# Kernel optimization log

Hardware: AMD Instinct MI355X
Metric: run time of the kernel (lower is better)

The kernel has to match this reference:

```python
import jax, jax.numpy as jnp
import numpy as np

D_MODEL = 1024
D_FF = 4096


def _layernorm(x, gamma, beta, eps=1e-5):
    mu = jnp.mean(x, axis=-1, keepdims=True)
    var = jnp.var(x, axis=-1, keepdims=True)
    return (x - mu) * jax.lax.rsqrt(var + eps) * gamma + beta


def setup_inputs() -> dict:
    key = jax.random.key(0)
    ks = jax.random.split(key, 7)
    B, S = 4, 2048
    src = jax.random.normal(ks[0], (B, S, D_MODEL), dtype=jnp.float32)
    gamma1 = jnp.ones((D_MODEL,), jnp.float32)
    beta1 = jnp.zeros((D_MODEL,), jnp.float32)
    gamma2 = jnp.ones((D_MODEL,), jnp.float32)
    beta2 = jnp.zeros((D_MODEL,), jnp.float32)
    w1 = jax.random.normal(ks[1], (D_MODEL, D_FF), jnp.float32) * (1.0 / np.sqrt(D_MODEL))
    b1 = jnp.zeros((D_FF,), jnp.float32)
    w2 = jax.random.normal(ks[2], (D_FF, D_MODEL), jnp.float32) * (1.0 / np.sqrt(D_FF))
    b2 = jnp.zeros((D_MODEL,), jnp.float32)
    return {"src": src, "gamma1": gamma1, "beta1": beta1,
            "gamma2": gamma2, "beta2": beta2,
            "w1": w1, "b1": b1, "w2": w2, "b2": b2}


def reference(src, gamma1, beta1, gamma2, beta2, w1, b1, w2, b2):
    # Pre-LN self-attention (single head, Q=K=V=norm_x, no projections)
    norm_x = _layernorm(src, gamma1, beta1)
    dim_k = norm_x.shape[-1]
    scores = jnp.einsum('bqd,bkd->bqk', norm_x, norm_x) / jnp.sqrt(jnp.float32(dim_k))
    weights = jax.nn.softmax(scores, axis=-1)
    attn = jnp.einsum('bqk,bkd->bqd', weights, norm_x)
    x = src + attn  # dropout p=0 -> identity
    # Pre-LN FFN
    h = _layernorm(x, gamma2, beta2)
    h = jax.nn.gelu(h @ w1 + b1, approximate=False)
    h = h @ w2 + b2
    return h + x
```

## Files before the change

### kernel.cpp

```cpp
#include <hip/hip_runtime.h>
#include <hip/hip_bf16.h>
#include <math.h>

typedef __attribute__((ext_vector_type(8))) short s8vec;
typedef __attribute__((ext_vector_type(16))) float f32x16;
typedef __attribute__((ext_vector_type(4))) unsigned short us4;
typedef __attribute__((ext_vector_type(2))) unsigned short us2;

__device__ __forceinline__ unsigned short f2bf(float f) {
  unsigned u = __float_as_uint(f);
  u = (u + 0x7fffu + ((u >> 16) & 1u)) >> 16;
  return (unsigned short)u;
}
__device__ __forceinline__ float bf2f(unsigned short u) {
  return __uint_as_float(((unsigned)u) << 16);
}

__device__ __forceinline__ float fast_gelu(float t) {
  float t2 = t * t;
  float u = t * (1.59576912f + 0.07135481f * t2);
  float e = __expf(-u);
  return t * __frcp_rn(1.0f + e);
}

__device__ __forceinline__ void async_ld16(const unsigned short* g, unsigned short* l) {
  __builtin_amdgcn_global_load_lds(
      (__attribute__((address_space(1))) void*)g,
      (__attribute__((address_space(3))) void*)l, 16, 0, 0);
}

template <int EPI>
__global__ __launch_bounds__(256) void gemm_nt(
    const unsigned short* __restrict__ A, const unsigned short* __restrict__ B,
    float* __restrict__ outF, unsigned short* __restrict__ outB,
    const float* __restrict__ bias, const float* __restrict__ res,
    int M, int N, int K,
    long long bA, long long bB, long long bO, long long bR, float scale)
{
  __shared__ __align__(16) unsigned short As[128 * 64];
  __shared__ __align__(16) unsigned short Bs[128 * 64];

  const int tid = threadIdx.x;
  const int w = tid >> 6;
  const int l = tid & 63;
  const int z = blockIdx.z;

  A += (size_t)z * bA;
  B += (size_t)z * bB;

  const size_t tileM = (size_t)blockIdx.y * 128;
  const size_t tileN = (size_t)blockIdx.x * 128;

  const int sRow = l >> 3;
  const unsigned short* aP[4];
  const unsigned short* bP[4];
#pragma unroll
  for (int i = 0; i < 4; ++i) {
    const int c = (l & 7) ^ sRow ^ i;
    aP[i] = A + (tileM + (w << 5) + (i << 3) + sRow) * (size_t)K + (c << 3);
    bP[i] = B + (tileN + (w << 5) + (i << 3) + sRow) * (size_t)K + (c << 3);
  }
  unsigned short* ldsA = &As[(w << 5) * 64];
  unsigned short* ldsB = &Bs[(w << 5) * 64];

  const int wm = (w >> 1) << 6;
  const int wn = (w & 1) << 6;
  const int fr = l & 31;
  const int fq = l >> 5;
  const int swz = (l & 7) ^ ((l >> 3) & 3);
  const int aRow = (wm + fr) * 64;
  const int bRow = (wn + fr) * 64;

  f32x16 acc[2][2] = {};

  for (int k0 = 0; k0 < K; k0 += 64) {
    __syncthreads();
#pragma unroll
    for (int i = 0; i < 4; ++i) {
      async_ld16(aP[i] + k0, ldsA + (i << 3) * 64);
      async_ld16(bP[i] + k0, ldsB + (i << 3) * 64);
    }
    __syncthreads();

#pragma unroll
    for (int s = 0; s < 4; ++s) {
      const int p = ((s << 1) + fq) ^ swz;
      s8vec af[2], bf[2];
#pragma unroll
      for (int i = 0; i < 2; ++i)
        af[i] = *(const s8vec*)&As[aRow + (i << 11) + (p << 3)];
#pragma unroll
      for (int j = 0; j < 2; ++j)
        bf[j] = *(const s8vec*)&Bs[bRow + (j << 11) + (p << 3)];
#pragma unroll
      for (int i = 0; i < 2; ++i)
#pragma unroll
        for (int j = 0; j < 2; ++j)
          acc[i][j] = __builtin_amdgcn_mfma_f32_32x32x16_bf16(af[i], bf[j], acc[i][j], 0, 0, 0);
    }
  }

  float* oF = outF + (size_t)z * bO;
  unsigned short* oB = outB + (size_t)z * bO;
  const float* rs = res + (size_t)z * bR;

  float bcol[2];
  if (EPI >= 2) {
#pragma unroll
    for (int j = 0; j < 2; ++j) bcol[j] = bias[tileN + wn + (j << 5) + fr];
  }

#pragma unroll
  for (int i = 0; i < 2; ++i) {
#pragma unroll
    for (int r = 0; r < 16; ++r) {
      const size_t row = tileM + wm + (i << 5) + (r & 3) + ((r >> 2) << 3) + (fq << 2);
      const size_t rb = row * (size_t)N;
#pragma unroll
      for (int j = 0; j < 2; ++j) {
        const size_t col = tileN + wn + (j << 5) + fr;
        const float v = acc[i][j][r];
        if (EPI == 0) {
          oB[rb + col] = f2bf(v * scale);
        } else if (EPI == 1) {
          oF[rb + col] = v + rs[rb + col];
        } else if (EPI == 2) {
          oB[rb + col] = f2bf(fast_gelu(v + bcol[j]));
        } else {
          oF[rb + col] = v + bcol[j] + rs[rb + col];
        }
      }
    }
  }
}

template <int EPI>
__global__ __launch_bounds__(256) void gemm_nt64(
    const unsigned short* __restrict__ A, const unsigned short* __restrict__ B,
    float* __restrict__ outF,
    const float* __restrict__ bias, const float* __restrict__ res,
    int M, int N, int K,
    long long bA, long long bB, long long bO, long long bR)
{
  __shared__ __align__(16) unsigned short As[64 * 64];
  __shared__ __align__(16) unsigned short Bs[128 * 64];

  const int tid = threadIdx.x;
  const int w = tid >> 6;
  const int l = tid & 63;
  const int z = blockIdx.z;

  A += (size_t)z * bA;
  B += (size_t)z * bB;

  const size_t tileM = (size_t)blockIdx.y * 64;
  const size_t tileN = (size_t)blockIdx.x * 128;

  const int sRow = l >> 3;
  const unsigned short* aP[2];
  const unsigned short* bP[4];
#pragma unroll
  for (int i = 0; i < 2; ++i) {
    const int gi = (w << 1) + i;
    const int c = (l & 7) ^ sRow ^ (gi & 3);
    aP[i] = A + (tileM + (gi << 3) + sRow) * (size_t)K + (c << 3);
  }
#pragma unroll
  for (int i = 0; i < 4; ++i) {
    const int gi = (w << 2) + i;
    const int c = (l & 7) ^ sRow ^ (gi & 3);
    bP[i] = B + (tileN + (gi << 3) + sRow) * (size_t)K + (c << 3);
  }
  unsigned short* ldsA = &As[(w << 1) * 512];
  unsigned short* ldsB = &Bs[(w << 2) * 512];

  const int wm = (w >> 1) << 5;
  const int wn = (w & 1) << 6;
  const int fr = l & 31;
  const int fq = l >> 5;
  const int swz = (l & 7) ^ ((l >> 3) & 3);
  const int aRow = (wm + fr) * 64;
  const int bRow = (wn + fr) * 64;

  f32x16 acc[2] = {};

  for (int k0 = 0; k0 < K; k0 += 64) {
    __syncthreads();
#pragma unroll
    for (int i = 0; i < 2; ++i)
      async_ld16(aP[i] + k0, ldsA + (i << 9));
#pragma unroll
    for (int i = 0; i < 4; ++i)
      async_ld16(bP[i] + k0, ldsB + (i << 9));
    __syncthreads();

#pragma unroll
    for (int s = 0; s < 4; ++s) {
      const int p = ((s << 1) + fq) ^ swz;
      s8vec af, bf[2];
      af = *(const s8vec*)&As[aRow + (p << 3)];
#pragma unroll
      for (int j = 0; j < 2; ++j)
        bf[j] = *(const s8vec*)&Bs[bRow + (j << 11) + (p << 3)];
#pragma unroll
      for (int j = 0; j < 2; ++j)
        acc[j] = __builtin_amdgcn_mfma_f32_32x32x16_bf16(af, bf[j], acc[j], 0, 0, 0);
    }
  }

  float* oF = outF + (size_t)z * bO;
  const float* rs = res + (size_t)z * bR;

  float bcol[2];
  if (EPI == 3) {
#pragma unroll
    for (int j = 0; j < 2; ++j) bcol[j] = bias[tileN + wn + (j << 5) + fr];
  }

#pragma unroll
  for (int r = 0; r < 16; ++r) {
    const size_t row = tileM + wm + (r & 3) + ((r >> 2) << 3) + (fq << 2);
    const size_t rb = row * (size_t)N;
#pragma unroll
    for (int j = 0; j < 2; ++j) {
      const size_t col = tileN + wn + (j << 5) + fr;
      const float v = acc[j][r];
      if (EPI == 1) {
        oF[rb + col] = v + rs[rb + col];
      } else {
        oF[rb + col] = v + bcol[j] + rs[rb + col];
      }
    }
  }
}

__global__ __launch_bounds__(256) void ln_row(
    const float* __restrict__ x, const float* __restrict__ gamma,
    const float* __restrict__ beta, unsigned short* __restrict__ out)
{
  const int row = blockIdx.x;
  const float4* xr = (const float4*)(x + (size_t)row * 1024);
  const int tid = threadIdx.x;
  float4 v = xr[tid];
  float s = v.x + v.y + v.z + v.w;
  float q = v.x * v.x + v.y * v.y + v.z * v.z + v.w * v.w;
#pragma unroll
  for (int off = 32; off > 0; off >>= 1) {
    s += __shfl_down(s, off);
    q += __shfl_down(q, off);
  }
  __shared__ float rs_[4], rq_[4];
  const int w = tid >> 6, l = tid & 63;
  if (l == 0) { rs_[w] = s; rq_[w] = q; }
  __syncthreads();
  s = rs_[0] + rs_[1] + rs_[2] + rs_[3];
  q = rq_[0] + rq_[1] + rq_[2] + rq_[3];
  const float mu = s * (1.0f / 1024.0f);
  const float var = q * (1.0f / 1024.0f) - mu * mu;
  const float rstd = rsqrtf(var + 1e-5f);
  const float4 g = ((const float4*)gamma)[tid];
  const float4 b = ((const float4*)beta)[tid];
  us4 o;
  o.x = f2bf((v.x - mu) * rstd * g.x + b.x);
  o.y = f2bf((v.y - mu) * rstd * g.y + b.y);
  o.z = f2bf((v.z - mu) * rstd * g.z + b.z);
  o.w = f2bf((v.w - mu) * rstd * g.w + b.w);
  ((us4*)(out + (size_t)row * 1024))[tid] = o;
}

__global__ __launch_bounds__(256) void softmax_row(
    const unsigned short* __restrict__ sc, unsigned short* __restrict__ pr)
{
  const int row = blockIdx.x;
  const s8vec* s8 = (const s8vec*)(sc + (size_t)row * 2048);
  const int tid = threadIdx.x;
  s8vec a = s8[tid];
  float x[8];
#pragma unroll
  for (int i = 0; i < 8; ++i) x[i] = bf2f((unsigned short)a[i]);
  float mx = x[0];
#pragma unroll
  for (int i = 1; i < 8; ++i) mx = fmaxf(mx, x[i]);
#pragma unroll
  for (int off = 32; off > 0; off >>= 1) mx = fmaxf(mx, __shfl_down(mx, off));
  __shared__ float red[4];
  const int w = tid >> 6, l = tid & 63;
  if (l == 0) red[w] = mx;
  __syncthreads();
  mx = fmaxf(fmaxf(red[0], red[1]), fmaxf(red[2], red[3]));
  __syncthreads();
  float e[8], s = 0.f;
#pragma unroll
  for (int i = 0; i < 8; ++i) { e[i] = __expf(x[i] - mx); s += e[i]; }
#pragma unroll
  for (int off = 32; off > 0; off >>= 1) s += __shfl_down(s, off);
  if (l == 0) red[w] = s;
  __syncthreads();
  s = red[0] + red[1] + red[2] + red[3];
  const float inv = 1.0f / s;
  s8vec o;
#pragma unroll
  for (int i = 0; i < 8; ++i) o[i] = (short)f2bf(e[i] * inv);
  ((s8vec*)(pr + (size_t)row * 2048))[tid] = o;
}

__global__ __launch_bounds__(256) void transpose_f32(
    const float* __restrict__ in, unsigned short* __restrict__ out, int R, int C)
{
  __shared__ float tile[64][33];
  const int tx = threadIdx.x, ty = threadIdx.y;
  const int c0 = blockIdx.x * 32, r0 = blockIdx.y * 64;
#pragma unroll
  for (int i = 0; i < 8; ++i) {
    const int rr = (ty << 3) + i;
    tile[rr][tx] = in[(size_t)(r0 + rr) * C + c0 + tx];
  }
  __syncthreads();
#pragma unroll
  for (int i = 0; i < 4; ++i) {
    const int oc = (ty << 2) + i;
    us2 v;
    v.x = f2bf(tile[2 * tx][oc]);
    v.y = f2bf(tile[2 * tx + 1][oc]);
    *(us2*)&out[(size_t)(c0 + oc) * R + r0 + 2 * tx] = v;
  }
}

__global__ __launch_bounds__(256) void transpose_bf16(
    const unsigned short* __restrict__ in_, unsigned short* __restrict__ out_,
    int R, int C, long long bIn, long long bOut)
{
  __shared__ float tile[32][33];
  const int z = blockIdx.z;
  const int tx = threadIdx.x, ty = threadIdx.y;
  const int c0 = blockIdx.x * 32, r0 = blockIdx.y * 32;
  const unsigned short* in = in_ + (size_t)z * bIn;
  for (int i = ty; i < 32; i += 8)
    tile[i][tx] = bf2f(in[(size_t)(r0 + i) * C + c0 + tx]);
  __syncthreads();
  unsigned short* o = out_ + (size_t)z * bOut;
  for (int i = ty; i < 32; i += 8)
    o[(size_t)(c0 + i) * R + r0 + tx] = f2bf(tile[tx][i]);
}

extern "C" void kernel_launch(void* const* d_in, const int* in_sizes, int n_in,
                              void* d_out, int out_size, void* d_ws, size_t ws_size,
                              hipStream_t stream)
{
  (void)in_sizes; (void)n_in; (void)out_size; (void)ws_size;
  const float* src = (const float*)d_in[0];
  const float* g1  = (const float*)d_in[1];
  const float* be1 = (const float*)d_in[2];
  const float* g2  = (const float*)d_in[3];
  const float* be2 = (const float*)d_in[4];
  const float* w1  = (const float*)d_in[5];
  const float* b1  = (const float*)d_in[6];
  const float* w2  = (const float*)d_in[7];
  const float* b2  = (const float*)d_in[8];
  float* out = (float*)d_out;

  char* ws = (char*)d_ws;
  const size_t SZ_NORMX  = (size_t)8192 * 1024 * 2;
  const size_t SZ_SCORES = (size_t)4 * 2048 * 2048 * 4;
  const size_t SZ_PROBS  = (size_t)4 * 2048 * 2048 * 2;
  const size_t SZ_X      = (size_t)8192 * 1024 * 4;
  const size_t SZ_W1T    = (size_t)1024 * 4096 * 2;

  unsigned short* normx  = (unsigned short*)(ws);
  unsigned short* normxT = (unsigned short*)(ws + SZ_NORMX);
  unsigned short* scores = (unsigned short*)(ws + 2 * SZ_NORMX);
  unsigned short* probs  = (unsigned short*)(ws + 2 * SZ_NORMX + SZ_SCORES);
  float*          xbuf   = (float*)(ws + 2 * SZ_NORMX + SZ_SCORES + SZ_PROBS);
  unsigned short* w1t    = (unsigned short*)(ws + 2 * SZ_NORMX + SZ_SCORES + SZ_PROBS + SZ_X);
  unsigned short* w2t    = (unsigned short*)(ws + 2 * SZ_NORMX + SZ_SCORES + SZ_PROBS + SZ_X + SZ_W1T);
  unsigned short* normx2 = normx;
  unsigned short* hbuf   = scores;

  transpose_f32<<<dim3(128, 16), dim3(32, 8), 0, stream>>>(w1, w1t, 1024, 4096);
  transpose_f32<<<dim3(32, 64), dim3(32, 8), 0, stream>>>(w2, w2t, 4096, 1024);

  ln_row<<<8192, 256, 0, stream>>>(src, g1, be1, normx);
  transpose_bf16<<<dim3(32, 64, 4), dim3(32, 8), 0, stream>>>(
      normx, normxT, 2048, 1024, (long long)2048 * 1024, (long long)1024 * 2048);

  gemm_nt<0><<<dim3(16, 16, 4), 256, 0, stream>>>(
      normx, normx, nullptr, scores, nullptr, nullptr,
      2048, 2048, 1024,
      (long long)2048 * 1024, (long long)2048 * 1024, (long long)2048 * 2048, 0, 0.03125f);

  softmax_row<<<8192, 256, 0, stream>>>(scores, probs);

  gemm_nt64<1><<<dim3(8, 32, 4), 256, 0, stream>>>(
      probs, normxT, xbuf, nullptr, src,
      2048, 1024, 2048,
      (long long)2048 * 2048, (long long)1024 * 2048, (long long)2048 * 1024,
      (long long)2048 * 1024);

  ln_row<<<8192, 256, 0, stream>>>(xbuf, g2, be2, normx2);

  gemm_nt<2><<<dim3(32, 64, 1), 256, 0, stream>>>(
      normx2, w1t, nullptr, hbuf, b1, nullptr,
      8192, 4096, 1024, 0, 0, 0, 0, 1.0f);

  gemm_nt64<3><<<dim3(8, 128, 1), 256, 0, stream>>>(
      hbuf, w2t, out, b2, xbuf,
      8192, 1024, 4096, 0, 0, 0, 0);
}
```

Before: 449.6 us.

## Route PV GEMM to larger-tile kernel and remap FFN2 blocks per XCD

The attention PV GEMM now uses the larger-tile gemm_nt kernel instead of the 64-row variant, halving the grid along M and increasing per-block reuse. The second FFN GEMM becomes a dedicated kernel with a 1D grid whose block index is remapped so each XCD gets a contiguous band of 16 row tiles and iterates across N tiles, improving L2 locality of the A operand. This trades occupancy/wave count for better reuse and cache behavior.

```diff
diff --git a/kernel.cpp b/kernel.cpp
--- a/kernel.cpp
+++ b/kernel.cpp
@@ -134,13 +134,11 @@
   }
 }
 
-template <int EPI>
-__global__ __launch_bounds__(256) void gemm_nt64(
+__global__ __launch_bounds__(256) void gemm_ffn2(
     const unsigned short* __restrict__ A, const unsigned short* __restrict__ B,
     float* __restrict__ outF,
     const float* __restrict__ bias, const float* __restrict__ res,
-    int M, int N, int K,
-    long long bA, long long bB, long long bO, long long bR)
+    int M, int N, int K)
 {
   __shared__ __align__(16) unsigned short As[64 * 64];
   __shared__ __align__(16) unsigned short Bs[128 * 64];
@@ -148,13 +146,12 @@
   const int tid = threadIdx.x;
   const int w = tid >> 6;
   const int l = tid & 63;
-  const int z = blockIdx.z;
-
-  A += (size_t)z * bA;
-  B += (size_t)z * bB;
-
-  const size_t tileM = (size_t)blockIdx.y * 64;
-  const size_t tileN = (size_t)blockIdx.x * 128;
+
+  const int bid = blockIdx.x;
+  const int xcd = bid & 7;
+  const int s0 = bid >> 3;
+  const size_t tileM = (size_t)((xcd << 4) | (s0 & 15)) * 64;
+  const size_t tileN = (size_t)(s0 >> 4) * 128;
 
   const int sRow = l >> 3;
   const unsigned short* aP[2];
@@ -208,14 +205,9 @@
     }
   }
 
-  float* oF = outF + (size_t)z * bO;
-  const float* rs = res + (size_t)z * bR;
-
   float bcol[2];
-  if (EPI == 3) {
-#pragma unroll
-    for (int j = 0; j < 2; ++j) bcol[j] = bias[tileN + wn + (j << 5) + fr];
-  }
+#pragma unroll
+  for (int j = 0; j < 2; ++j) bcol[j] = bias[tileN + wn + (j << 5) + fr];
 
 #pragma unroll
   for (int r = 0; r < 16; ++r) {
@@ -224,12 +216,7 @@
 #pragma unroll
     for (int j = 0; j < 2; ++j) {
       const size_t col = tileN + wn + (j << 5) + fr;
-      const float v = acc[j][r];
-      if (EPI == 1) {
-        oF[rb + col] = v + rs[rb + col];
-      } else {
-        oF[rb + col] = v + bcol[j] + rs[rb + col];
-      }
+      outF[rb + col] = acc[j][r] + bcol[j] + res[rb + col];
     }
   }
 }
@@ -390,11 +377,11 @@
 
   softmax_row<<<8192, 256, 0, stream>>>(scores, probs);
 
-  gemm_nt64<1><<<dim3(8, 32, 4), 256, 0, stream>>>(
-      probs, normxT, xbuf, nullptr, src,
+  gemm_nt<1><<<dim3(8, 16, 4), 256, 0, stream>>>(
+      probs, normxT, xbuf, nullptr, nullptr, src,
       2048, 1024, 2048,
       (long long)2048 * 2048, (long long)1024 * 2048, (long long)2048 * 1024,
-      (long long)2048 * 1024);
+      (long long)2048 * 1024, 1.0f);
 
   ln_row<<<8192, 256, 0, stream>>>(xbuf, g2, be2, normx2);
 
@@ -402,7 +389,6 @@
       normx2, w1t, nullptr, hbuf, b1, nullptr,
       8192, 4096, 1024, 0, 0, 0, 0, 1.0f);
 
-  gemm_nt64<3><<<dim3(8, 128, 1), 256, 0, stream>>>(
-      hbuf, w2t, out, b2, xbuf,
-      8192, 1024, 4096, 0, 0, 0, 0);
-}
+  gemm_ffn2<<<1024, 256, 0, stream>>>(
+      hbuf, w2t, out, b2, xbuf, 8192, 1024, 4096);
+}
```

Result: faster. 431.4 us (-4.0%).
